# Kernel tuning notes

Measured on AMD Instinct MI355X. Metric: run time of the kernel, lower is better.

Reference implementation:

```python
import jax, jax.numpy as jnp
import numpy as np

N, G, K = 16384, 32, 8          # cells, hvg genes (32*32 covet), n_neighs
IN_DIM, HID, OUT = 2000, 1024, 30


def setup_inputs() -> dict:
    key = jax.random.key(0)
    ks = jax.random.split(key, 8)
    return {
        "x": jax.random.normal(ks[0], (N, IN_DIM), jnp.float32),
        "coordinates": jax.random.uniform(ks[1], (N, 2), jnp.float32) * 100.0,
        "highly_variable_genes": jax.random.uniform(ks[2], (N, G), jnp.float32),
        # fc1: Linear(input_dim + 32*32, hidden); stored as [in, out]
        "W1": jax.random.normal(ks[3], (IN_DIM + G * G, HID), jnp.float32) * 0.02,
        "b1": jnp.zeros((HID,), jnp.float32),
        "W2": jax.random.normal(ks[4], (HID, OUT), jnp.float32) * 0.02,
        "b2": jnp.zeros((OUT,), jnp.float32),
    }


def _covet_sqrt(genes, coords, k):
    # brute-force kNN over spatial coordinates (squared euclidean)
    sq = jnp.sum(coords * coords, axis=1)                      # [N]
    d2 = sq[:, None] + sq[None, :] - 2.0 * (coords @ coords.T)  # [N, N]
    _, idx = jax.lax.top_k(-d2, k)                             # [N, k] nearest (incl. self)
    neigh = genes[idx]                                         # [N, k, G] irregular gather
    # COVET: center neighborhoods at the GLOBAL mean expression
    centered = neigh - jnp.mean(genes, axis=0)                 # [N, k, G]
    cov = jnp.einsum('nkg,nkh->ngh', centered, centered) / (k - 1)  # [N, G, G]
    # matrix square root of each PSD covariance via eigh
    w, V = jnp.linalg.eigh(cov)
    s = jnp.sqrt(jnp.clip(w, 0.0, None))                       # [N, G]
    return jnp.einsum('ngk,nk,nhk->ngh', V, s, V)              # V diag(s) V^T


def reference(x, coordinates, highly_variable_genes, W1, b1, W2, b2):
    # original runs covet_sqrt in numpy -> detached from autograd
    covet = jax.lax.stop_gradient(
        _covet_sqrt(highly_variable_genes, coordinates, K))
    hidden = jnp.concatenate([x, covet.reshape(-1, G * G)], axis=1)  # [N, IN+1024]
    h = jax.nn.relu(hidden @ W1 + b1)
    return h @ W2 + b2
```

## Files before the change

### kernel.cpp

```cpp
#include <hip/hip_runtime.h>
#include <hip/hip_bf16.h>
#include <math.h>

#define N_CELLS 16384
#define G_GENES 32
#define IN_DIM  2000
#define HID     1024
#define OUT_DIM 30
#define K_TOT   3024
#define K_PAD   3040
#define NT      95
#define GRID_B  128
#define NBINS   (GRID_B * GRID_B)
#define SCELL   (100.0f / (float)GRID_B)
#define CSCALE  0.37796447300922722721f

typedef unsigned short ushort_t;
typedef __attribute__((ext_vector_type(8))) short bf16x8;
typedef __attribute__((ext_vector_type(4))) short bf16x4;
typedef __attribute__((ext_vector_type(4))) float f32x4;

__device__ __forceinline__ ushort_t f2bf(float v) {
  return __builtin_bit_cast(ushort_t, __float2bfloat16(v));
}

__device__ __forceinline__ void glds16(const void* g, void* l) {
  __builtin_amdgcn_global_load_lds(
      (const __attribute__((address_space(1))) unsigned int*)g,
      (__attribute__((address_space(3))) unsigned int*)l, 16, 0, 0);
}

__global__ __launch_bounds__(256) void fused_pre(const float* __restrict__ x,
                                                 const float* __restrict__ W1,
                                                 const float* __restrict__ W2,
                                                 const float* __restrict__ genes,
                                                 const float* __restrict__ coords,
                                                 ushort_t* __restrict__ Abf,
                                                 ushort_t* __restrict__ Bh,
                                                 ushort_t* __restrict__ W2t,
                                                 double* __restrict__ part,
                                                 int* __restrict__ cnt,
                                                 int* __restrict__ binOf) {
  __shared__ float L[32][260];
  __shared__ double red[256];
  const int bid = blockIdx.x;
  const int tid = threadIdx.x;

  if (bid < 380) {
    const int cb = bid / NT, t = bid % NT;
    const int k0 = t * 32, n0 = cb * 256;
    {
      const int kl = tid >> 3;
      const int nw = tid & 7;
#pragma unroll
      for (int u = 0; u < 8; ++u) {
        const int nl = (nw + u * 8) * 4;
        float4 v = make_float4(0.f, 0.f, 0.f, 0.f);
        if (k0 + kl < K_TOT) v = *(const float4*)(W1 + (size_t)(k0 + kl) * HID + n0 + nl);
        L[kl][nl + 0] = v.x; L[kl][nl + 1] = v.y; L[kl][nl + 2] = v.z; L[kl][nl + 3] = v.w;
      }
    }
    __syncthreads();
    const size_t tileBase = ((size_t)cb * NT + t) * 8192;
    const int n = tid;
#pragma unroll
    for (int q = 0; q < 4; ++q) {
      const int cdata = q ^ ((n >> 1) & 3);
      ushort_t hi[8];
#pragma unroll
      for (int e = 0; e < 8; ++e) {
        const int kl = cdata * 8 + e;
        const float v = (k0 + kl < K_TOT) ? L[kl][n] : 0.f;
        hi[e] = f2bf(v);
      }
      *(bf16x8*)(Bh + tileBase + ((size_t)n * 4 + q) * 8) = *(const bf16x8*)hi;
    }
  } else if (bid < 384) {
    const int k = (bid - 380) * 256 + tid;
#pragma unroll
    for (int o = 0; o < 32; ++o) {
      const float v = (o < OUT_DIM) ? W2[k * OUT_DIM + o] : 0.f;
      W2t[o * HID + k] = f2bf(v);
    }
  } else if (bid < 2432) {
    const int rbase = (bid - 384) * 8;
#pragma unroll
    for (int rr = 0; rr < 8; ++rr) {
      const int row = rbase + rr;
      if (tid < 250) {
#pragma unroll
        for (int ph = 0; ph < 2; ++ph) {
          const int col = ph * 1000 + tid * 4;
          const float4 v = *(const float4*)(x + (size_t)row * IN_DIM + col);
          ushort_t o[4] = { f2bf(v.x), f2bf(v.y), f2bf(v.z), f2bf(v.w) };
          *(bf16x4*)(Abf + (size_t)row * K_PAD + col) = *(const bf16x4*)o;
        }
      } else if (tid < 252) {
        const bf16x8 z = (bf16x8){0, 0, 0, 0, 0, 0, 0, 0};
        *(bf16x8*)(Abf + (size_t)row * K_PAD + K_TOT + (tid - 250) * 8) = z;
      }
    }
  } else if (bid < 2560) {
    const int b = bid - 2432;
    const int g = tid & 31, cs = tid >> 5;
    double acc = 0.0;
#pragma unroll
    for (int it = 0; it < 16; ++it) {
      const int cell = b * 128 + cs + it * 8;
      acc += (double)genes[cell * G_GENES + g];
    }
    red[tid] = acc;
    __syncthreads();
    if (tid < 32) {
      double s = red[tid];
#pragma unroll
      for (int u = 1; u < 8; ++u) s += red[tid + u * 32];
      part[b * 32 + tid] = s;
    }
  } else {
    const int i = (bid - 2560) * 256 + tid;
    const float2 p = ((const float2*)coords)[i];
    const float inv_s = (float)GRID_B / 100.0f;
    const int bx = min(GRID_B - 1, max(0, (int)(p.x * inv_s)));
    const int by = min(GRID_B - 1, max(0, (int)(p.y * inv_s)));
    const int b = by * GRID_B + bx;
    binOf[i] = b;
    atomicAdd(&cnt[b], 1);
  }
}

__global__ __launch_bounds__(256) void scan_fin(const int* __restrict__ cnt,
                                                int* __restrict__ binStart,
                                                int* __restrict__ cursor,
                                                const double* __restrict__ part,
                                                float* __restrict__ meanv) {
  const int tid = threadIdx.x;
  if (blockIdx.x == 0) {
    __shared__ int ps[256];
    int s = 0;
    for (int i = 0; i < 64; ++i) s += cnt[tid * 64 + i];
    ps[tid] = s;
    __syncthreads();
    for (int off = 1; off < 256; off <<= 1) {
      const int add = (tid >= off) ? ps[tid - off] : 0;
      __syncthreads();
      ps[tid] += add;
      __syncthreads();
    }
    int run = ps[tid] - s;
    for (int i = 0; i < 64; ++i) {
      const int b = tid * 64 + i;
      binStart[b] = run;
      cursor[b] = run;
      run += cnt[b];
    }
    if (tid == 255) binStart[NBINS] = run;
  } else {
    if (tid < 32) {
      double s = 0.0;
      for (int b = 0; b < 128; ++b) s += part[b * 32 + tid];
      meanv[tid] = (float)(s / (double)N_CELLS);
    }
  }
}

__global__ __launch_bounds__(256) void bin_scatter(const float* __restrict__ coords,
                                                   const int* __restrict__ binOf,
                                                   int* __restrict__ cursor,
                                                   int* __restrict__ binPts,
                                                   float2* __restrict__ sxy) {
  const int i = blockIdx.x * 256 + threadIdx.x;
  const float2 p = ((const float2*)coords)[i];
  const int pos = atomicAdd(&cursor[binOf[i]], 1);
  binPts[pos] = i;
  sxy[pos] = p;
}

__global__ __launch_bounds__(128) void knn_search(const int* __restrict__ binStart,
                                                  const int* __restrict__ binPts,
                                                  const float2* __restrict__ sxy,
                                                  int* __restrict__ nidx) {
  const int rank = blockIdx.x * 128 + threadIdx.x;
  const int cell = binPts[rank];
  const float2 qv = sxy[rank];
  const float qx = qv.x, qy = qv.y;
  const float sqi = __fadd_rn(__fmul_rn(qx, qx), __fmul_rn(qy, qy));
  const float inv_s = (float)GRID_B / 100.0f;
  const int bx = min(GRID_B - 1, max(0, (int)(qx * inv_s)));
  const int by = min(GRID_B - 1, max(0, (int)(qy * inv_s)));

  unsigned long long kk[8];
#pragma unroll
  for (int i = 0; i < 8; ++i) kk[i] = ~0ull;

  auto scan_seg = [&](int s, int e) {
    for (int p = s; p < e; ++p) {
      const float2 pc = sxy[p];
      const int j = binPts[p];
      const float sqj = __fadd_rn(__fmul_rn(pc.x, pc.x), __fmul_rn(pc.y, pc.y));
      const float dot = __fmaf_rn(qy, pc.y, __fmul_rn(qx, pc.x));
      const float d2  = __fsub_rn(__fadd_rn(sqi, sqj), __fmul_rn(2.0f, dot));
      unsigned int sb = __float_as_uint(d2);
      sb = (sb & 0x80000000u) ? ~sb : (sb | 0x80000000u);
      unsigned long long key = ((unsigned long long)sb << 32) | (unsigned int)j;
      if (key < kk[7]) {
#pragma unroll
        for (int q2 = 0; q2 < 8; ++q2) {
          const bool lt = key < kk[q2];
          const unsigned long long tmp = kk[q2];
          kk[q2] = lt ? key : kk[q2];
          key = lt ? tmp : key;
        }
      }
    }
  };

  bool done = false;
  for (int r = 0; r < GRID_B; ++r) {
    if (!done) {
      if (r == 0) {
        const int b = by * GRID_B + bx;
        scan_seg(binStart[b], binStart[b + 1]);
      } else {
        const int xlo = max(0, bx - r), xhi = min(GRID_B - 1, bx + r);
        if (by - r >= 0) {
          const int b0 = (by - r) * GRID_B;
          scan_seg(binStart[b0 + xlo], binStart[b0 + xhi + 1]);
        }
        if (by + r < GRID_B) {
          const int b0 = (by + r) * GRID_B;
          scan_seg(binStart[b0 + xlo], binStart[b0 + xhi + 1]);
        }
        for (int dy = -r + 1; dy <= r - 1; ++dy) {
          const int yy = by + dy;
          if (yy < 0 || yy >= GRID_B) continue;
          if (bx - r >= 0) { const int b = yy * GRID_B + bx - r; scan_seg(binStart[b], binStart[b + 1]); }
          if (bx + r < GRID_B) { const int b = yy * GRID_B + bx + r; scan_seg(binStart[b], binStart[b + 1]); }
        }
      }
      if (kk[7] != ~0ull) {
        const unsigned int sb = (unsigned int)(kk[7] >> 32);
        const float wd2 = __uint_as_float((sb & 0x80000000u) ? (sb ^ 0x80000000u) : ~sb);
        const float bnd = (float)r * SCELL;
        if (wd2 < bnd * bnd * 0.998f - 0.05f) done = true;
      }
    }
    if (!__any(!done)) break;
  }
#pragma unroll
  for (int i = 0; i < 8; ++i) nidx[cell * 8 + i] = (int)(kk[i] & 0xFFFFFFFFu);
}

__global__ __launch_bounds__(256) void gram_kernel(const float* __restrict__ genes,
                                                   const float* __restrict__ meanv,
                                                   const int* __restrict__ nidx,
                                                   float* __restrict__ GwsT) {
  const int wv = threadIdx.x >> 6, lane = threadIdx.x & 63;
  const int bidl = (blockIdx.x & 7) * 512 + (blockIdx.x >> 3);
  const int cell = bidl * 4 + wv;
  __shared__ float A[4][8][33];
#pragma unroll
  for (int q = 0; q < 4; ++q) {
    const int e = lane + (q << 6);
    const int n = e >> 5, g = e & 31;
    const int src = nidx[cell * 8 + n];
    A[wv][n][g] = (genes[src * G_GENES + g] - meanv[g]) * CSCALE;
  }
  __syncthreads();
  const int i = lane >> 3, j = lane & 7;
  float acc = 0.f;
#pragma unroll
  for (int g = 0; g < 32; ++g) acc = fmaf(A[wv][i][g], A[wv][j][g], acc);
  GwsT[(size_t)lane * N_CELLS + cell] = acc;
}

__global__ __launch_bounds__(64) void jacobi_kernel(const float* __restrict__ GwsT,
                                                    float* __restrict__ VwsT,
                                                    float* __restrict__ lamT) {
  const int cell = blockIdx.x * 64 + threadIdx.x;
  float Gm[8][8], V[8][8];
#pragma unroll
  for (int e = 0; e < 64; ++e) Gm[e >> 3][e & 7] = GwsT[(size_t)e * N_CELLS + cell];
#pragma unroll
  for (int i = 0; i < 8; ++i)
#pragma unroll
    for (int j = 0; j < 8; ++j) V[i][j] = (i == j) ? 1.0f : 0.0f;

  for (int sweep = 0; sweep < 6; ++sweep) {
#pragma unroll
    for (int p = 0; p < 7; ++p) {
#pragma unroll
      for (int q = p + 1; q < 8; ++q) {
        const float apq = Gm[p][q];
        const float app = Gm[p][p], aqq = Gm[q][q];
        float t;
        if (apq != 0.0f) {
          const float tau = (aqq - app) / (2.0f * apq);
          const float r = sqrtf(fmaf(tau, tau, 1.0f));
          t = copysignf(1.0f, tau) / (fabsf(tau) + r);
        } else {
          t = 0.0f;
        }
        const float c = 1.0f / sqrtf(fmaf(t, t, 1.0f));
        const float s = t * c;
#pragma unroll
        for (int r2 = 0; r2 < 8; ++r2) {
          const float gp = Gm[p][r2], gq = Gm[q][r2];
          Gm[p][r2] = fmaf(c, gp, -s * gq);
          Gm[q][r2] = fmaf(s, gp,  c * gq);
        }
#pragma unroll
        for (int r2 = 0; r2 < 8; ++r2) {
          const float gp = Gm[r2][p], gq = Gm[r2][q];
          Gm[r2][p] = fmaf(c, gp, -s * gq);
          Gm[r2][q] = fmaf(s, gp,  c * gq);
        }
#pragma unroll
        for (int r2 = 0; r2 < 8; ++r2) {
          const float vp = V[r2][p], vq = V[r2][q];
          V[r2][p] = fmaf(c, vp, -s * vq);
          V[r2][q] = fmaf(s, vp,  c * vq);
        }
      }
    }
  }
#pragma unroll
  for (int e = 0; e < 64; ++e) VwsT[(size_t)e * N_CELLS + cell] = V[e >> 3][e & 7];
#pragma unroll
  for (int m = 0; m < 8; ++m) lamT[(size_t)m * N_CELLS + cell] = Gm[m][m];
}

__global__ __launch_bounds__(256) void recon_kernel(const float* __restrict__ genes,
                                                    const float* __restrict__ meanv,
                                                    const int* __restrict__ nidx,
                                                    const float* __restrict__ VwsT,
                                                    const float* __restrict__ lamT,
                                                    ushort_t* __restrict__ Abf) {
  const int wv = threadIdx.x >> 6, lane = threadIdx.x & 63;
  const int cell = blockIdx.x * 4 + wv;
  __shared__ float A[4][8][33];
  __shared__ float Ws[4][8][33];
  __shared__ float Vs[4][64];
  __shared__ float lamS[4][8];
#pragma unroll
  for (int q = 0; q < 4; ++q) {
    const int e = lane + (q << 6);
    const int n = e >> 5, g = e & 31;
    const int src = nidx[cell * 8 + n];
    A[wv][n][g] = (genes[src * G_GENES + g] - meanv[g]) * CSCALE;
  }
  Vs[wv][lane] = VwsT[(size_t)lane * N_CELLS + cell];
  if (lane < 8) lamS[wv][lane] = lamT[(size_t)lane * N_CELLS + cell];
  __syncthreads();

  float maxl = 0.f;
#pragma unroll
  for (int m = 0; m < 8; ++m) maxl = fmaxf(maxl, lamS[wv][m]);
  const float thr = maxl * 1e-8f;

#pragma unroll
  for (int q = 0; q < 4; ++q) {
    const int e = lane + (q << 6);
    const int m = e >> 5, g = e & 31;
    float acc = 0.f;
#pragma unroll
    for (int i = 0; i < 8; ++i) acc = fmaf(Vs[wv][i * 8 + m], A[wv][i][g], acc);
    const float l = lamS[wv][m];
    const float scm = (l > thr) ? sqrtf(1.0f / sqrtf(l)) : 0.0f;
    Ws[wv][m][g] = acc * scm;
  }
  __syncthreads();
  ushort_t* dst = Abf + (size_t)cell * K_PAD + IN_DIM;
#pragma unroll
  for (int r = 0; r < 16; ++r) {
    const int o = (r << 6) + lane;
    const int g = o >> 5, hh = o & 31;
    float acc = 0.f;
#pragma unroll
    for (int m = 0; m < 8; ++m) acc = fmaf(Ws[wv][m][g], Ws[wv][m][hh], acc);
    dst[o] = f2bf(acc);
  }
}

__global__ __launch_bounds__(512, 4) void gemm1_kernel(const ushort_t* __restrict__ Abf,
                                                       const ushort_t* __restrict__ Bh,
                                                       const float* __restrict__ b1,
                                                       ushort_t* __restrict__ h) {
  __shared__ ushort_t As[4][4096];
  __shared__ ushort_t Bs[3][8192];

  const int tid = threadIdx.x;
  const int id  = blockIdx.x;
  const int xcd = id & 7, local = id >> 3;
  const int rb  = (xcd << 4) + (local & 15);
  const int cb  = local >> 4;
  const int row0 = rb << 7, col0 = cb << 8;

  const int lane = tid & 63, wv = tid >> 6;
  const int m_base = (wv >> 2) << 6, n_base = (wv & 3) << 6;
  const int l15 = lane & 15, l4 = lane >> 4;

  const int arow = tid >> 2, acpos = tid & 3;
  const int acdata = acpos ^ ((arow >> 1) & 3);
  const ushort_t* aptr = Abf + (size_t)(row0 + arow) * K_PAD + acdata * 8;
  const ushort_t* bptr = Bh + (size_t)cb * NT * 8192 + tid * 8;

  int aoff[4], boff[4];
#pragma unroll
  for (int i = 0; i < 4; ++i) {
    const int r = m_base + i * 16 + l15;
    aoff[i] = r * 32 + (l4 ^ ((r >> 1) & 3)) * 8;
  }
#pragma unroll
  for (int j = 0; j < 4; ++j) {
    const int r = n_base + j * 16 + l15;
    boff[j] = r * 32 + (l4 ^ ((r >> 1) & 3)) * 8;
  }

  f32x4 acc[4][4];
#pragma unroll
  for (int i = 0; i < 4; ++i)
#pragma unroll
    for (int j = 0; j < 4; ++j) acc[i][j] = (f32x4){0.f, 0.f, 0.f, 0.f};

  auto gldsA = [&](int buf) {
    glds16(aptr, &As[buf][tid * 8]);
    aptr += 32;
  };
  auto gldsB = [&](int buf) {
    glds16(bptr,        &Bs[buf][tid * 8]);
    glds16(bptr + 4096, &Bs[buf][tid * 8 + 4096]);
    bptr += 8192;
  };
  auto compute = [&](int ab, int bb) {
    bf16x8 ah[4], bh[4];
#pragma unroll
    for (int i = 0; i < 4; ++i) ah[i] = *(const bf16x8*)(&As[ab][aoff[i]]);
#pragma unroll
    for (int j = 0; j < 4; ++j) bh[j] = *(const bf16x8*)(&Bs[bb][boff[j]]);
#pragma unroll
    for (int i = 0; i < 4; ++i)
#pragma unroll
      for (int j = 0; j < 4; ++j)
        acc[i][j] = __builtin_amdgcn_mfma_f32_16x16x32_bf16(ah[i], bh[j], acc[i][j], 0, 0, 0);
  };

  gldsA(0); gldsB(0);
  gldsA(1); gldsB(1);
  gldsA(2);
  asm volatile("s_waitcnt vmcnt(4)" ::: "memory");
  __builtin_amdgcn_s_barrier();
  __builtin_amdgcn_sched_barrier(0);

  for (int t = 0; t < 92; ++t) {
    gldsB((t + 2) % 3);
    gldsA((t + 3) & 3);
    compute(t & 3, t % 3);
    asm volatile("s_waitcnt vmcnt(4)" ::: "memory");
    __builtin_amdgcn_s_barrier();
    __builtin_amdgcn_sched_barrier(0);
  }
  gldsB(94 % 3);
  compute(92 & 3, 92 % 3);
  asm volatile("s_waitcnt vmcnt(3)" ::: "memory");
  __builtin_amdgcn_s_barrier();
  __builtin_amdgcn_sched_barrier(0);
  compute(93 & 3, 93 % 3);
  asm volatile("s_waitcnt vmcnt(0)" ::: "memory");
  __builtin_amdgcn_s_barrier();
  __builtin_amdgcn_sched_barrier(0);
  compute(94 & 3, 94 % 3);

  float bb[4];
#pragma unroll
  for (int j = 0; j < 4; ++j) bb[j] = b1[col0 + n_base + j * 16 + l15];
#pragma unroll
  for (int i = 0; i < 4; ++i) {
    const int rbase = row0 + m_base + i * 16 + l4 * 4;
#pragma unroll
    for (int j = 0; j < 4; ++j) {
      const int c = col0 + n_base + j * 16 + l15;
#pragma unroll
      for (int q = 0; q < 4; ++q) {
        const float v = fmaxf(acc[i][j][q] + bb[j], 0.f);
        h[(size_t)(rbase + q) * HID + c] = f2bf(v);
      }
    }
  }
}

__global__ __launch_bounds__(256) void gemm2_kernel(const ushort_t* __restrict__ h,
                                                    const ushort_t* __restrict__ W2t,
                                                    const float* __restrict__ b2,
                                                    float* __restrict__ out) {
  const int tid = threadIdx.x;
  const int lane = tid & 63, wv = tid >> 6;
  const int rowt = wv & 1, colt = wv >> 1;
  const int l15 = lane & 15, l4 = lane >> 4;
  const int row0 = blockIdx.x * 32 + rowt * 16;
  const int col  = colt * 16 + l15;

  f32x4 acc = (f32x4){0.f, 0.f, 0.f, 0.f};
  const ushort_t* ha = h + (size_t)(row0 + l15) * HID + l4 * 8;
  const ushort_t* wb = W2t + (size_t)col * HID + l4 * 8;
#pragma unroll 8
  for (int k0 = 0; k0 < HID; k0 += 32) {
    const bf16x8 av = *(const bf16x8*)(ha + k0);
    const bf16x8 bv = *(const bf16x8*)(wb + k0);
    acc = __builtin_amdgcn_mfma_f32_16x16x32_bf16(av, bv, acc, 0, 0, 0);
  }
  if (col < OUT_DIM) {
    const float bias = b2[col];
#pragma unroll
    for (int q = 0; q < 4; ++q) {
      const int r = row0 + l4 * 4 + q;
      out[(size_t)r * OUT_DIM + col] = acc[q] + bias;
    }
  }
}

extern "C" void kernel_launch(void* const* d_in, const int* in_sizes, int n_in,
                              void* d_out, int out_size, void* d_ws, size_t ws_size,
                              hipStream_t stream) {
  (void)in_sizes; (void)n_in; (void)out_size;
  const float* x      = (const float*)d_in[0];
  const float* coords = (const float*)d_in[1];
  const float* genes  = (const float*)d_in[2];
  const float* W1     = (const float*)d_in[3];
  const float* b1     = (const float*)d_in[4];
  const float* W2     = (const float*)d_in[5];
  const float* b2     = (const float*)d_in[6];
  float* out = (float*)d_out;

  char* ws = (char*)d_ws;
  size_t off = 0;
  auto alloc = [&](size_t bytes) -> void* {
    void* p = ws + off;
    off = (off + bytes + 255) & ~(size_t)255;
    return p;
  };
  ushort_t* Abf    = (ushort_t*)alloc((size_t)N_CELLS * K_PAD * 2);
  ushort_t* hbf    = (ushort_t*)alloc((size_t)N_CELLS * HID * 2);
  ushort_t* Bh     = (ushort_t*)alloc((size_t)4 * NT * 8192 * 2);
  ushort_t* W2t    = (ushort_t*)alloc((size_t)32 * HID * 2);
  float*    GwsT   = (float*)alloc((size_t)64 * N_CELLS * 4);
  float*    VwsT   = (float*)alloc((size_t)64 * N_CELLS * 4);
  float*    lamT   = (float*)alloc((size_t)8 * N_CELLS * 4);
  int*      nidx   = (int*)alloc((size_t)N_CELLS * 8 * 4);
  double*   part   = (double*)alloc((size_t)128 * 32 * 8);
  float*    meanv  = (float*)alloc(G_GENES * 4);
  int*      binCnt = (int*)alloc((size_t)NBINS * 4);
  int*      binSt  = (int*)alloc((size_t)(NBINS + 1) * 4);
  int*      cursor = (int*)alloc((size_t)NBINS * 4);
  int*      binOf  = (int*)alloc((size_t)N_CELLS * 4);
  int*      binPts = (int*)alloc((size_t)N_CELLS * 4);
  float2*   sxy    = (float2*)alloc((size_t)N_CELLS * 8);
  if (off > ws_size) return;

  hipMemsetAsync(binCnt, 0, (size_t)NBINS * 4, stream);

  hipLaunchKernelGGL(fused_pre,   dim3(2624),  dim3(256), 0, stream,
                     x, W1, W2, genes, coords, Abf, Bh, W2t, part, binCnt, binOf);
  hipLaunchKernelGGL(scan_fin,    dim3(2),     dim3(256), 0, stream, binCnt, binSt, cursor, part, meanv);
  hipLaunchKernelGGL(bin_scatter, dim3(64),    dim3(256), 0, stream, coords, binOf, cursor, binPts, sxy);
  hipLaunchKernelGGL(knn_search,  dim3(128),   dim3(128), 0, stream, binSt, binPts, sxy, nidx);
  hipLaunchKernelGGL(gram_kernel, dim3(4096),  dim3(256), 0, stream, genes, meanv, nidx, GwsT);
  hipLaunchKernelGGL(jacobi_kernel, dim3(256), dim3(64),  0, stream, GwsT, VwsT, lamT);
  hipLaunchKernelGGL(recon_kernel,  dim3(4096), dim3(256), 0, stream, genes, meanv, nidx, VwsT, lamT, Abf);
  hipLaunchKernelGGL(gemm1_kernel,  dim3(512),  dim3(512), 0, stream, Abf, Bh, b1, hbf);
  hipLaunchKernelGGL(gemm2_kernel,  dim3(512),  dim3(256), 0, stream, hbf, W2t, b2, out);
}
```

Measured before the change: 287.3 us.

## Stream GEMM1 B tiles from global into registers instead of LDS

```diff
diff --git a/kernel.cpp b/kernel.cpp
--- a/kernel.cpp
+++ b/kernel.cpp
@@ -382,12 +382,11 @@
   }
 }
 
-__global__ __launch_bounds__(512, 4) void gemm1_kernel(const ushort_t* __restrict__ Abf,
+__global__ __launch_bounds__(512, 3) void gemm1_kernel(const ushort_t* __restrict__ Abf,
                                                        const ushort_t* __restrict__ Bh,
                                                        const float* __restrict__ b1,
                                                        ushort_t* __restrict__ h) {
-  __shared__ ushort_t As[4][4096];
-  __shared__ ushort_t Bs[3][8192];
+  __shared__ ushort_t As[3][4096];
 
   const int tid = threadIdx.x;
   const int id  = blockIdx.x;
@@ -403,73 +402,85 @@
   const int arow = tid >> 2, acpos = tid & 3;
   const int acdata = acpos ^ ((arow >> 1) & 3);
   const ushort_t* aptr = Abf + (size_t)(row0 + arow) * K_PAD + acdata * 8;
-  const ushort_t* bptr = Bh + (size_t)cb * NT * 8192 + tid * 8;
-
-  int aoff[4], boff[4];
+
+  const ushort_t* bbase = Bh + (size_t)cb * NT * 8192;
+  int boffg[4];
+#pragma unroll
+  for (int j = 0; j < 4; ++j) {
+    const int r = n_base + j * 16 + l15;
+    boffg[j] = (r * 4 + (l4 ^ ((r >> 1) & 3))) * 8;
+  }
+  int aoff[4];
 #pragma unroll
   for (int i = 0; i < 4; ++i) {
     const int r = m_base + i * 16 + l15;
     aoff[i] = r * 32 + (l4 ^ ((r >> 1) & 3)) * 8;
   }
-#pragma unroll
-  for (int j = 0; j < 4; ++j) {
-    const int r = n_base + j * 16 + l15;
-    boff[j] = r * 32 + (l4 ^ ((r >> 1) & 3)) * 8;
-  }
 
   f32x4 acc[4][4];
 #pragma unroll
   for (int i = 0; i < 4; ++i)
 #pragma unroll
     for (int j = 0; j < 4; ++j) acc[i][j] = (f32x4){0.f, 0.f, 0.f, 0.f};
+
+  float4 rB0[4], rB1[4];
 
   auto gldsA = [&](int buf) {
     glds16(aptr, &As[buf][tid * 8]);
     aptr += 32;
   };
-  auto gldsB = [&](int buf) {
-    glds16(bptr,        &Bs[buf][tid * 8]);
-    glds16(bptr + 4096, &Bs[buf][tid * 8 + 4096]);
-    bptr += 8192;
+  auto loadB = [&](int t, float4* rb) {
+    const ushort_t* p = bbase + (size_t)t * 8192;
+#pragma unroll
+    for (int j = 0; j < 4; ++j) rb[j] = *(const float4*)(p + boffg[j]);
   };
-  auto compute = [&](int ab, int bb) {
-    bf16x8 ah[4], bh[4];
+  auto compute = [&](int ab, const float4* rb) {
+    bf16x8 ah[4];
 #pragma unroll
     for (int i = 0; i < 4; ++i) ah[i] = *(const bf16x8*)(&As[ab][aoff[i]]);
 #pragma unroll
-    for (int j = 0; j < 4; ++j) bh[j] = *(const bf16x8*)(&Bs[bb][boff[j]]);
-#pragma unroll
     for (int i = 0; i < 4; ++i)
 #pragma unroll
       for (int j = 0; j < 4; ++j)
-        acc[i][j] = __builtin_amdgcn_mfma_f32_16x16x32_bf16(ah[i], bh[j], acc[i][j], 0, 0, 0);
+        acc[i][j] = __builtin_amdgcn_mfma_f32_16x16x32_bf16(
+            ah[i], __builtin_bit_cast(bf16x8, rb[j]), acc[i][j], 0, 0, 0);
   };
 
-  gldsA(0); gldsB(0);
-  gldsA(1); gldsB(1);
-  gldsA(2);
-  asm volatile("s_waitcnt vmcnt(4)" ::: "memory");
-  __builtin_amdgcn_s_barrier();
-  __builtin_amdgcn_sched_barrier(0);
-
-  for (int t = 0; t < 92; ++t) {
-    gldsB((t + 2) % 3);
-    gldsA((t + 3) & 3);
-    compute(t & 3, t % 3);
-    asm volatile("s_waitcnt vmcnt(4)" ::: "memory");
-    __builtin_amdgcn_s_barrier();
-    __builtin_amdgcn_sched_barrier(0);
-  }
-  gldsB(94 % 3);
-  compute(92 & 3, 92 % 3);
-  asm volatile("s_waitcnt vmcnt(3)" ::: "memory");
-  __builtin_amdgcn_s_barrier();
-  __builtin_amdgcn_sched_barrier(0);
-  compute(93 & 3, 93 % 3);
+#define WAIT1() { asm volatile("s_waitcnt vmcnt(1)" ::: "memory"); \
+                  __builtin_amdgcn_s_barrier(); \
+                  __builtin_amdgcn_sched_barrier(0); }
+
+  loadB(0, rB0);
+  gldsA(0);
+  gldsA(1);
+  WAIT1();
+
+  for (int tp = 0; tp < 46; ++tp) {
+    const int t0 = 2 * tp;
+    {
+      loadB(t0 + 1, rB1);
+      gldsA((t0 + 2) % 3);
+      compute(t0 % 3, rB0);
+      WAIT1();
+    }
+    {
+      loadB(t0 + 2, rB0);
+      gldsA((t0 + 3) % 3);
+      compute((t0 + 1) % 3, rB1);
+      WAIT1();
+    }
+  }
+  loadB(93, rB1);
+  gldsA(94 % 3);
+  compute(92 % 3, rB0);
+  WAIT1();
+  loadB(94, rB0);
+  compute(93 % 3, rB1);
   asm volatile("s_waitcnt vmcnt(0)" ::: "memory");
   __builtin_amdgcn_s_barrier();
   __builtin_amdgcn_sched_barrier(0);
-  compute(94 & 3, 94 % 3);
+  compute(94 % 3, rB0);
+#undef WAIT1
 
   float bb[4];
 #pragma unroll
```

Result: slower. 388.0 us (+35.1%).
